# Optimization experiments

Measured on AMD Instinct MI355X. Metric: run time of the kernel, lower is better.

## Reference

```python
import jax, jax.numpy as jnp
from jax import lax
import numpy as np

B, DIM, H, W = 4, 64, 256, 256
HEADS = 8
# (pad_h, pad_w) for kernels (1,7),(1,11),(1,21),(7,1),(11,1),(21,1)
PADS = [(0, 3), (0, 5), (0, 10), (3, 0), (5, 0), (10, 0)]
KSHAPES = [(1, 7), (1, 11), (1, 21), (7, 1), (11, 1), (21, 1)]


def _ln(x, w, b):
    # LayerNorm over channel dim per pixel (torch does it in 'b (h w) c' layout)
    mu = jnp.mean(x, axis=1, keepdims=True)
    var = jnp.mean((x - mu) ** 2, axis=1, keepdims=True)  # unbiased=False
    return (x - mu) / jnp.sqrt(var + 1e-5) * w[None, :, None, None] + b[None, :, None, None]


def _dw(x, k, b, pad):
    # depthwise conv, k: (dim, 1, kh, kw)
    y = lax.conv_general_dilated(
        x, k, window_strides=(1, 1),
        padding=[(pad[0], pad[0]), (pad[1], pad[1])],
        feature_group_count=k.shape[0],
        dimension_numbers=('NCHW', 'OIHW', 'NCHW'))
    return y + b[None, :, None, None]


def _pw(x, w, b):
    # 1x1 conv
    return jnp.einsum('oc,bchw->bohw', w, x) + b[None, :, None, None]


def _l2n(x):
    # torch F.normalize(dim=-1): x / max(||x||_2, 1e-12)
    n = jnp.sqrt(jnp.sum(x * x, axis=-1, keepdims=True))
    return x / jnp.maximum(n, 1e-12)


def _to_attn(t, b, h, w, cph):
    # 'b (head c) h w -> b head w (h c)'  (h slow, c fast in last dim)
    t = t.reshape(b, HEADS, cph, h, w)
    return t.transpose(0, 1, 4, 3, 2).reshape(b, HEADS, w, h * cph)


def setup_inputs() -> dict:
    key = jax.random.key(0)
    keys = jax.random.split(key, 16)
    inp = {
        'x1': jax.random.normal(keys[0], (B, DIM, H, W), jnp.float32),
        'x2': jax.random.normal(keys[1], (B, DIM, H, W), jnp.float32),
        'ln1_w': jnp.ones((DIM,), jnp.float32),
        'ln1_b': jnp.zeros((DIM,), jnp.float32),
        'ln2_w': jnp.ones((DIM,), jnp.float32),
        'ln2_b': jnp.zeros((DIM,), jnp.float32),
        'b_dw': jnp.zeros((12, DIM), jnp.float32),
        'w_pw': 0.05 * jax.random.normal(keys[2], (DIM, DIM), jnp.float32),
        'b_pw': jnp.zeros((DIM,), jnp.float32),
    }
    names = ['k11', 'k12', 'k13', 'k14', 'k15', 'k16',
             'k21', 'k22', 'k23', 'k24', 'k25', 'k26']
    for i, nm in enumerate(names):
        kh, kw = KSHAPES[i % 6]
        inp[nm] = 0.1 * jax.random.normal(keys[3 + i], (DIM, 1, kh, kw), jnp.float32)
    return inp


def reference(x1, x2, ln1_w, ln1_b, ln2_w, ln2_b,
              k11, k12, k13, k14, k15, k16,
              k21, k22, k23, k24, k25, k26,
              b_dw, w_pw, b_pw):
    b, c, h, w = x2.shape
    cph = c // HEADS
    x1n = _ln(x1, ln1_w, ln1_b)
    x2n = _ln(x2, ln2_w, ln2_b)
    ks1 = (k11, k12, k13, k14, k15, k16)
    ks2 = (k21, k22, k23, k24, k25, k26)
    out1 = sum(_dw(x1n, k, b_dw[i], PADS[i]) for i, k in enumerate(ks1))
    out2 = sum(_dw(x2n, k, b_dw[6 + i], PADS[i]) for i, k in enumerate(ks2))
    out1 = _pw(out1, w_pw, b_pw)  # shared 1x1 conv (same weights for both)
    out2 = _pw(out2, w_pw, b_pw)
    q = _l2n(_to_attn(out1, b, h, w, cph))   # (b, head, w, h*cph)
    kk = _l2n(_to_attn(out2, b, h, w, cph))
    v = _to_attn(out2, b, h, w, cph)
    attn = jax.nn.softmax(jnp.einsum('bnwd,bnvd->bnwv', q, kk), axis=-1)
    out4 = jnp.einsum('bnwv,bnvd->bnwd', attn, v) + q
    out4 = out4.reshape(b, HEADS, w, h, cph).transpose(0, 1, 4, 3, 2).reshape(b, c, h, w)
    # note: torch rebinds x1/x2 to normalized tensors before the residual add
    return _pw(out4, w_pw, b_pw) + x1n + x2n
```

## Files before the change

### kernel.cpp

```cpp
#include <hip/hip_runtime.h>

#define HW 65536

typedef __bf16 bf16x8 __attribute__((ext_vector_type(8)));
typedef float f32x4 __attribute__((ext_vector_type(4)));

__device__ __forceinline__ float b2f(unsigned short u) {
    return __uint_as_float(((unsigned)u) << 16);
}
__device__ __forceinline__ unsigned short f2bu(float f) {
    unsigned u = __float_as_uint(f);
    return (unsigned short)((u + 0x7FFFu + ((u >> 16) & 1u)) >> 16);
}
__device__ __forceinline__ void up2(unsigned u, float& lo, float& hi) {
    lo = __uint_as_float(u << 16);
    hi = __uint_as_float(u & 0xFFFF0000u);
}

__global__ void k_prep(const float* k11, const float* k12, const float* k13,
                       const float* k14, const float* k15, const float* k16,
                       const float* k21, const float* k22, const float* k23,
                       const float* k24, const float* k25, const float* k26,
                       const float* bdw, float* wcomb, float* bias) {
    int c = threadIdx.x;
    if (c >= 64) return;
    float* wh1 = wcomb;
    float* wv1 = wcomb + 1344;
    float* wh2 = wcomb + 2688;
    float* wv2 = wcomb + 4032;
    for (int j = 0; j < 21; j++) {
        wh1[c*21+j] = k13[c*21+j];
        wv1[c*21+j] = k16[c*21+j];
        wh2[c*21+j] = k23[c*21+j];
        wv2[c*21+j] = k26[c*21+j];
    }
    for (int j = 0; j < 11; j++) {
        wh1[c*21+j+5] += k12[c*11+j];
        wv1[c*21+j+5] += k15[c*11+j];
        wh2[c*21+j+5] += k22[c*11+j];
        wv2[c*21+j+5] += k25[c*11+j];
    }
    for (int j = 0; j < 7; j++) {
        wh1[c*21+j+7] += k11[c*7+j];
        wv1[c*21+j+7] += k14[c*7+j];
        wh2[c*21+j+7] += k21[c*7+j];
        wv2[c*21+j+7] += k24[c*7+j];
    }
    float s1 = 0.f, s2 = 0.f;
    for (int i = 0; i < 6; i++) { s1 += bdw[i*64+c]; s2 += bdw[(6+i)*64+c]; }
    bias[c] = s1; bias[64+c] = s2;
}

__global__ __launch_bounds__(256) void k_ln(
        const float* __restrict__ x1, const float* __restrict__ x2,
        const float* __restrict__ w1, const float* __restrict__ b1,
        const float* __restrict__ w2, const float* __restrict__ b2,
        unsigned short* __restrict__ o1, unsigned short* __restrict__ o2,
        unsigned short* __restrict__ s12) {
    int p = blockIdx.x * 256 + threadIdx.x;
    int b = p >> 16, hw = p & (HW - 1);
    size_t base = (size_t)b * 64 * HW + hw;
    float v[64];
    unsigned n1[32];
    {
        float s = 0.f;
        #pragma unroll
        for (int c = 0; c < 64; c++) { v[c] = x1[base + (size_t)c * HW]; s += v[c]; }
        float mu = s * 0.015625f, s2 = 0.f;
        #pragma unroll
        for (int c = 0; c < 64; c++) { float d = v[c] - mu; s2 += d * d; }
        float rstd = rsqrtf(s2 * 0.015625f + 1e-5f);
        #pragma unroll
        for (int c2 = 0; c2 < 32; c2++) {
            unsigned short lo = f2bu((v[2*c2]   - mu) * rstd * w1[2*c2]   + b1[2*c2]);
            unsigned short hi = f2bu((v[2*c2+1] - mu) * rstd * w1[2*c2+1] + b1[2*c2+1]);
            o1[base + (size_t)(2*c2)   * HW] = lo;
            o1[base + (size_t)(2*c2+1) * HW] = hi;
            n1[c2] = (unsigned)lo | ((unsigned)hi << 16);
        }
    }
    {
        float s = 0.f;
        #pragma unroll
        for (int c = 0; c < 64; c++) { v[c] = x2[base + (size_t)c * HW]; s += v[c]; }
        float mu = s * 0.015625f, s2 = 0.f;
        #pragma unroll
        for (int c = 0; c < 64; c++) { float d = v[c] - mu; s2 += d * d; }
        float rstd = rsqrtf(s2 * 0.015625f + 1e-5f);
        #pragma unroll
        for (int c2 = 0; c2 < 32; c2++) {
            float a2 = (v[2*c2]   - mu) * rstd * w2[2*c2]   + b2[2*c2];
            float b2n = (v[2*c2+1] - mu) * rstd * w2[2*c2+1] + b2[2*c2+1];
            o2[base + (size_t)(2*c2)   * HW] = f2bu(a2);
            o2[base + (size_t)(2*c2+1) * HW] = f2bu(b2n);
            float lo, hi;
            up2(n1[c2], lo, hi);
            s12[base + (size_t)(2*c2)   * HW] = f2bu(lo + a2);
            s12[base + (size_t)(2*c2+1) * HW] = f2bu(hi + b2n);
        }
    }
}

__global__ __launch_bounds__(256) void k_dw(
        const unsigned short* __restrict__ in1, const unsigned short* __restrict__ in2,
        const float* __restrict__ wcomb, const float* __restrict__ bias,
        unsigned short* __restrict__ o1, unsigned short* __restrict__ o2) {
    __shared__ __align__(16) unsigned short tile[52][288];
    int which = blockIdx.y;
    const unsigned short* in = which ? in2 : in1;
    unsigned short* o = which ? o2 : o1;
    int bx = blockIdx.x;
    int bc = bx >> 3, tileid = bx & 7;
    int c = bc & 63;
    int h0 = tileid * 32;
    const float* whp = wcomb + which * 2688 + c * 21;
    const float* wvp = whp + 1344;
    float wh[21], wv[21];
    #pragma unroll
    for (int j = 0; j < 21; j++) { wh[j] = whp[j]; wv[j] = wvp[j]; }
    float bs = bias[which * 64 + c];
    const unsigned short* src = in + (size_t)bc * HW;
    int tid = threadIdx.x;

    for (int idx = tid; idx < 52 * 36; idx += 256) {
        int row = idx / 36, chunk = idx - row * 36;
        int grow = h0 - 10 + row;
        uint4 val = make_uint4(0u, 0u, 0u, 0u);
        if ((unsigned)grow < 256u && chunk >= 2 && chunk <= 33)
            val = *(const uint4*)(src + grow * 256 + (chunk - 2) * 8);
        *(uint4*)&tile[row][chunk * 8] = val;
    }
    __syncthreads();

    int seg = tid & 31, rgrp = tid >> 5;
    int w0 = seg * 8;
    int r0 = rgrp * 4;

    float acc[4][8];
    #pragma unroll
    for (int k = 0; k < 4; k++)
        #pragma unroll
        for (int i = 0; i < 8; i++) acc[k][i] = bs;

    #pragma unroll
    for (int rr = 0; rr < 24; rr++) {
        uint4 u = *(const uint4*)&tile[r0 + rr][16 + w0];
        float v[8];
        up2(u.x, v[0], v[1]); up2(u.y, v[2], v[3]);
        up2(u.z, v[4], v[5]); up2(u.w, v[6], v[7]);
        #pragma unroll
        for (int k = 0; k < 4; k++) {
            const int j = rr - k;
            if (j >= 0 && j < 21) {
                float wt = wv[j];
                #pragma unroll
                for (int i = 0; i < 8; i++) acc[k][i] += wt * v[i];
            }
        }
    }

    #pragma unroll
    for (int k = 0; k < 4; k++) {
        const unsigned short* rowp = &tile[r0 + k + 10][w0 + 4];
        float hv[32];
        #pragma unroll
        for (int q = 0; q < 8; q++) {
            uint2 u = *(const uint2*)(rowp + q * 4);
            up2(u.x, hv[q*4+0], hv[q*4+1]);
            up2(u.y, hv[q*4+2], hv[q*4+3]);
        }
        #pragma unroll
        for (int j = 0; j < 21; j++) {
            float wt = wh[j];
            #pragma unroll
            for (int i = 0; i < 8; i++) acc[k][i] += wt * hv[i + j + 2];
        }
    }

    size_t obase = (size_t)bc * HW;
    #pragma unroll
    for (int k = 0; k < 4; k++) {
        uint4 u;
        u.x = (unsigned)f2bu(acc[k][0]) | ((unsigned)f2bu(acc[k][1]) << 16);
        u.y = (unsigned)f2bu(acc[k][2]) | ((unsigned)f2bu(acc[k][3]) << 16);
        u.z = (unsigned)f2bu(acc[k][4]) | ((unsigned)f2bu(acc[k][5]) << 16);
        u.w = (unsigned)f2bu(acc[k][6]) | ((unsigned)f2bu(acc[k][7]) << 16);
        *(uint4*)(o + obase + (size_t)(h0 + r0 + k) * 256 + w0) = u;
    }
}

__global__ __launch_bounds__(256) void k_pw(
        const unsigned short* __restrict__ in1, const unsigned short* __restrict__ in2,
        const float* __restrict__ wpw, const float* __restrict__ bpw,
        unsigned short* __restrict__ Eq, unsigned short* __restrict__ Fk,
        unsigned short* __restrict__ Fv) {
    __shared__ __align__(16) unsigned short Ws[64][72];
    __shared__ __align__(16) unsigned short Xs[64][260];
    __shared__ float sb[64];
    int tid = threadIdx.x;
    for (int i = tid; i < 4096; i += 256) Ws[i >> 6][i & 63] = f2bu(wpw[i]);
    if (tid < 64) sb[tid] = bpw[tid];
    int which = blockIdx.y;
    const unsigned short* in = which ? in2 : in1;
    int bx = blockIdx.x;
    int b = bx & 3;
    int h = ((bx >> 2) & 31) * 8 + (bx >> 7);
    const unsigned short* src = in + (size_t)b * 64 * HW + h * 256;
    for (int i = tid; i < 2048; i += 256) {
        int c = i >> 5, ch = i & 31;
        uint4 u = *(const uint4*)(src + (size_t)c * HW + ch * 8);
        *(uint2*)&Xs[c][ch * 8]     = make_uint2(u.x, u.y);
        *(uint2*)&Xs[c][ch * 8 + 4] = make_uint2(u.z, u.w);
    }
    __syncthreads();

    int lane = tid & 63, wv = tid >> 6;
    int rA = lane & 15, g = lane >> 4;
    int p_off = wv * 64;

    f32x4 acc[4][4];
    #pragma unroll
    for (int m = 0; m < 4; m++)
        #pragma unroll
        for (int n = 0; n < 4; n++) acc[m][n] = (f32x4){0.f, 0.f, 0.f, 0.f};

    #pragma unroll
    for (int ks = 0; ks < 2; ks++) {
        int c0 = ks * 32;
        bf16x8 a[4], bb[4];
        #pragma unroll
        for (int m = 0; m < 4; m++)
            a[m] = *(const bf16x8*)&Ws[16 * m + rA][c0 + 8 * g];
        #pragma unroll
        for (int n = 0; n < 4; n++) {
            int p = p_off + 16 * n + rA;
            uint4 bu;
            bu.x = (unsigned)Xs[c0 + 8*g + 0][p] | ((unsigned)Xs[c0 + 8*g + 1][p] << 16);
            bu.y = (unsigned)Xs[c0 + 8*g + 2][p] | ((unsigned)Xs[c0 + 8*g + 3][p] << 16);
            bu.z = (unsigned)Xs[c0 + 8*g + 4][p] | ((unsigned)Xs[c0 + 8*g + 5][p] << 16);
            bu.w = (unsigned)Xs[c0 + 8*g + 6][p] | ((unsigned)Xs[c0 + 8*g + 7][p] << 16);
            bb[n] = *(bf16x8*)&bu;
        }
        #pragma unroll
        for (int m = 0; m < 4; m++)
            #pragma unroll
            for (int n = 0; n < 4; n++)
                acc[m][n] = __builtin_amdgcn_mfma_f32_16x16x32_bf16(a[m], bb[n], acc[m][n], 0, 0, 0);
    }

    unsigned short* dst = which ? Fk : Eq;
    size_t b8 = (size_t)b * 8;
    #pragma unroll
    for (int m = 0; m < 4; m++) {
        int o0 = 16 * m + 4 * g;
        int hd = o0 >> 3, cp = o0 & 7;
        #pragma unroll
        for (int n = 0; n < 4; n++) {
            int p = p_off + 16 * n + rA;
            ushort4 pk;
            #pragma unroll
            for (int r = 0; r < 4; r++)
                ((unsigned short*)&pk)[r] = f2bu(acc[m][n][r] + sb[o0 + r]);
            *(ushort4*)(dst + ((b8 + hd) * 256 + p) * 2048 + h * 8 + cp) = pk;
            if (which) {
                #pragma unroll
                for (int r = 0; r < 4; r++) {
                    int o = o0 + r;
                    Fv[((b8 + (o >> 3)) * 2048 + h * 8 + (o & 7)) * 256 + p] =
                        ((unsigned short*)&pk)[r];
                }
            }
        }
    }
}

__global__ __launch_bounds__(256) void k_norm(
        const unsigned short* __restrict__ Eq, const unsigned short* __restrict__ Fk,
        float* __restrict__ invQ, float* __restrict__ invK) {
    int lane = threadIdx.x & 63, wid = threadIdx.x >> 6;
    int row = blockIdx.x * 4 + wid;
    const unsigned short* src = (row < 8192) ? Eq : Fk;
    int r = row & 8191;
    const unsigned short* p = src + (size_t)r * 2048;
    float s = 0.f;
    #pragma unroll
    for (int it = 0; it < 4; it++) {
        uint4 u = *(const uint4*)(p + it * 512 + lane * 8);
        unsigned vals[4] = {u.x, u.y, u.z, u.w};
        #pragma unroll
        for (int e = 0; e < 4; e++) {
            float lo = b2f((unsigned short)(vals[e] & 0xffffu));
            float hi = b2f((unsigned short)(vals[e] >> 16));
            s += lo * lo + hi * hi;
        }
    }
    #pragma unroll
    for (int m = 1; m < 64; m <<= 1) s += __shfl_xor(s, m, 64);
    if (lane == 0) {
        float inv = 1.f / fmaxf(sqrtf(s), 1e-12f);
        (row < 8192 ? invQ : invK)[r] = inv;
    }
}

__global__ __launch_bounds__(512, 4) void k_qkt(
        const unsigned short* __restrict__ Eq, const unsigned short* __restrict__ Fk,
        float* __restrict__ Sp) {
    int bx = blockIdx.x;
    int bh = bx & 31, t2 = bx >> 5;
    int itile = t2 >> 1, ks = t2 & 1;
    int i0 = itile * 32;
    const unsigned short* Q  = Eq + (size_t)bh * 524288 + ks * 1024;
    const unsigned short* Kp = Fk + (size_t)bh * 524288 + ks * 1024;
    int tid = threadIdx.x, lane = tid & 63, wid = tid >> 6;
    int rA = lane & 15, g = lane >> 4, kf = g * 8;

    f32x4 acc[2][2];
    #pragma unroll
    for (int ib = 0; ib < 2; ib++)
        #pragma unroll
        for (int jb = 0; jb < 2; jb++) acc[ib][jb] = (f32x4){0.f, 0.f, 0.f, 0.f};

    const unsigned short* q0  = Q  + (size_t)(i0 + rA) * 2048 + kf;
    const unsigned short* q1  = q0 + 16 * 2048;
    const unsigned short* kr0 = Kp + (size_t)(wid * 32 + rA) * 2048 + kf;
    const unsigned short* kr1 = kr0 + 16 * 2048;
    for (int k0 = 0; k0 < 1024; k0 += 128) {
        bf16x8 a0[4], a1[4], b0[4], b1[4];
        #pragma unroll
        for (int s = 0; s < 4; s++) {
            int kk = k0 + s * 32;
            a0[s] = *(const bf16x8*)(q0 + kk);
            a1[s] = *(const bf16x8*)(q1 + kk);
            b0[s] = *(const bf16x8*)(kr0 + kk);
            b1[s] = *(const bf16x8*)(kr1 + kk);
        }
        #pragma unroll
        for (int s = 0; s < 4; s++) {
            acc[0][0] = __builtin_amdgcn_mfma_f32_16x16x32_bf16(a0[s], b0[s], acc[0][0], 0, 0, 0);
            acc[1][0] = __builtin_amdgcn_mfma_f32_16x16x32_bf16(a1[s], b0[s], acc[1][0], 0, 0, 0);
            acc[0][1] = __builtin_amdgcn_mfma_f32_16x16x32_bf16(a0[s], b1[s], acc[0][1], 0, 0, 0);
            acc[1][1] = __builtin_amdgcn_mfma_f32_16x16x32_bf16(a1[s], b1[s], acc[1][1], 0, 0, 0);
        }
    }
    float* Sb = Sp + (size_t)(ks * 32 + bh) * 65536 + (size_t)i0 * 256;
    #pragma unroll
    for (int ib = 0; ib < 2; ib++)
        #pragma unroll
        for (int jb = 0; jb < 2; jb++)
            #pragma unroll
            for (int r = 0; r < 4; r++)
                Sb[(ib * 16 + g * 4 + r) * 256 + wid * 32 + jb * 16 + rA] = acc[ib][jb][r];
}

__global__ __launch_bounds__(256) void k_smx(
        const float* __restrict__ Sp, const float* __restrict__ invQ,
        const float* __restrict__ invK, unsigned short* __restrict__ P) {
    __shared__ float sKv[256];
    int bx = blockIdx.x;
    int bh = bx & 31, rg = bx >> 5;
    int tid = threadIdx.x;
    sKv[tid] = invK[bh * 256 + tid];
    __syncthreads();
    int lr = tid >> 5, sub = tid & 31;
    int i = rg * 8 + lr;
    int R = bh * 256 + i;
    const float* p0 = Sp + (size_t)bh * 65536 + i * 256;
    const float* p1 = Sp + (size_t)(32 + bh) * 65536 + i * 256;
    float qs = invQ[R];
    int c0 = sub * 8;
    float4 a0 = *(const float4*)(p0 + c0), a1 = *(const float4*)(p0 + c0 + 4);
    float4 b0 = *(const float4*)(p1 + c0), b1 = *(const float4*)(p1 + c0 + 4);
    float v[8];
    v[0] = (a0.x + b0.x); v[1] = (a0.y + b0.y); v[2] = (a0.z + b0.z); v[3] = (a0.w + b0.w);
    v[4] = (a1.x + b1.x); v[5] = (a1.y + b1.y); v[6] = (a1.z + b1.z); v[7] = (a1.w + b1.w);
    float m = -1e30f;
    #pragma unroll
    for (int e = 0; e < 8; e++) {
        v[e] *= qs * sKv[c0 + e];
        m = fmaxf(m, v[e]);
    }
    #pragma unroll
    for (int msk = 1; msk < 32; msk <<= 1) m = fmaxf(m, __shfl_xor(m, msk, 32));
    float s = 0.f;
    #pragma unroll
    for (int e = 0; e < 8; e++) { v[e] = __expf(v[e] - m); s += v[e]; }
    #pragma unroll
    for (int msk = 1; msk < 32; msk <<= 1) s += __shfl_xor(s, msk, 32);
    float inv = 1.f / s;
    uint4 w;
    w.x = (unsigned)f2bu(v[0] * inv) | ((unsigned)f2bu(v[1] * inv) << 16);
    w.y = (unsigned)f2bu(v[2] * inv) | ((unsigned)f2bu(v[3] * inv) << 16);
    w.z = (unsigned)f2bu(v[4] * inv) | ((unsigned)f2bu(v[5] * inv) << 16);
    w.w = (unsigned)f2bu(v[6] * inv) | ((unsigned)f2bu(v[7] * inv) << 16);
    *(uint4*)(P + (size_t)R * 256 + c0) = w;
}

__global__ __launch_bounds__(512, 4) void k_pv(
        const unsigned short* __restrict__ P, const unsigned short* __restrict__ Fv,
        const unsigned short* __restrict__ Eq, const float* __restrict__ invQ,
        unsigned short* __restrict__ G) {
    __shared__ __align__(16) unsigned short Pb[32][256];
    __shared__ __align__(16) unsigned short Qs[32][1024];
    __shared__ float sQ[32];
    int bx = blockIdx.x;
    int bh = bx & 31, t2 = bx >> 5;
    int itile = t2 >> 1, ds = t2 & 1;
    int i0 = itile * 32;
    int b = bh >> 3, hd = bh & 7;
    const unsigned short* Vt = Fv + (size_t)bh * 524288;
    int tid = threadIdx.x, lane = tid & 63, wid = tid >> 6;
    for (int i = tid; i < 1024; i += 512) {
        int r = i >> 5, cu = i & 31;
        uint4 u = *(const uint4*)(P + (size_t)(bh * 256 + i0 + r) * 256 + cu * 8);
        int su = cu ^ (r & 7);
        *(uint4*)&Pb[r][su * 8] = u;
    }
    for (int i = tid; i < 4096; i += 512) {
        int r = i >> 7, cu = i & 127;
        *(uint4*)&Qs[r][cu * 8] =
            *(const uint4*)(Eq + (size_t)(bh * 256 + i0 + r) * 2048 + ds * 1024 + cu * 8);
    }
    if (tid < 32) sQ[tid] = invQ[bh * 256 + i0 + tid];
    __syncthreads();

    int rA = lane & 15, g = lane >> 4, kf = g * 8;

    bf16x8 pa[2][8];
    #pragma unroll
    for (int ib = 0; ib < 2; ib++)
        #pragma unroll
        for (int ksl = 0; ksl < 8; ksl++) {
            int rr = ib * 16 + rA;
            int unit = (ksl * 4 + g) ^ (rr & 7);
            pa[ib][ksl] = *(const bf16x8*)&Pb[rr][unit * 8];
        }

    int dloc = wid * 128;
    for (int dt = 0; dt < 8; dt++) {
        int dl = dloc + dt * 16;
        int d0 = ds * 1024 + dl;
        const unsigned short* vp = Vt + (size_t)(d0 + rA) * 256 + kf;
        bf16x8 vb[8];
        #pragma unroll
        for (int ksl = 0; ksl < 8; ksl++)
            vb[ksl] = *(const bf16x8*)(vp + ksl * 32);
        f32x4 o0 = {0.f, 0.f, 0.f, 0.f}, o1 = {0.f, 0.f, 0.f, 0.f};
        #pragma unroll
        for (int ksl = 0; ksl < 8; ksl++) {
            o0 = __builtin_amdgcn_mfma_f32_16x16x32_bf16(pa[0][ksl], vb[ksl], o0, 0, 0, 0);
            o1 = __builtin_amdgcn_mfma_f32_16x16x32_bf16(pa[1][ksl], vb[ksl], o1, 0, 0, 0);
        }
        int d = d0 + rA;
        int dlr = dl + rA;
        int cpr = d & 7, hh = d >> 3;
        #pragma unroll
        for (int ib = 0; ib < 2; ib++) {
            f32x4 oa = ib ? o1 : o0;
            int ibase = i0 + ib * 16 + g * 4;
            ushort4 pk;
            #pragma unroll
            for (int r = 0; r < 4; r++) {
                int il = ib * 16 + g * 4 + r;
                float qv = b2f(Qs[il][dlr]) * sQ[il];
                ((unsigned short*)&pk)[r] = f2bu(oa[r] + qv);
            }
            *(ushort4*)(G + (size_t)(b * 64 + hd * 8 + cpr) * HW + hh * 256 + ibase) = pk;
        }
    }
}

__global__ __launch_bounds__(256) void k_final(
        const unsigned short* __restrict__ G, const unsigned short* __restrict__ S12g,
        const float* __restrict__ wpw, const float* __restrict__ bpw,
        float* __restrict__ out) {
    __shared__ __align__(16) unsigned short Ws[64][72];
    __shared__ __align__(16) unsigned short Gs[64][260];
    __shared__ __align__(16) unsigned short S12[64][260];
    __shared__ float sb[64];
    int tid = threadIdx.x;
    for (int i = tid; i < 4096; i += 256) Ws[i >> 6][i & 63] = f2bu(wpw[i]);
    if (tid < 64) sb[tid] = bpw[tid];
    int bx = blockIdx.x, b = bx >> 8, h = bx & 255;
    const unsigned short* src = G + (size_t)b * 64 * HW + h * 256;
    const unsigned short* ssrc = S12g + (size_t)b * 64 * HW + h * 256;
    for (int i = tid; i < 2048; i += 256) {
        int c = i >> 5, ch = i & 31;
        uint4 u = *(const uint4*)(src + (size_t)c * HW + ch * 8);
        *(uint2*)&Gs[c][ch * 8]     = make_uint2(u.x, u.y);
        *(uint2*)&Gs[c][ch * 8 + 4] = make_uint2(u.z, u.w);
        uint4 v = *(const uint4*)(ssrc + (size_t)c * HW + ch * 8);
        *(uint2*)&S12[c][ch * 8]     = make_uint2(v.x, v.y);
        *(uint2*)&S12[c][ch * 8 + 4] = make_uint2(v.z, v.w);
    }
    __syncthreads();

    int lane = tid & 63, wv = tid >> 6;
    int rA = lane & 15, g = lane >> 4;
    int p_off = wv * 64;

    f32x4 acc[4][4];
    #pragma unroll
    for (int m = 0; m < 4; m++)
        #pragma unroll
        for (int n = 0; n < 4; n++) acc[m][n] = (f32x4){0.f, 0.f, 0.f, 0.f};

    #pragma unroll
    for (int ks = 0; ks < 2; ks++) {
        int c0 = ks * 32;
        bf16x8 a[4], bb[4];
        #pragma unroll
        for (int m = 0; m < 4; m++)
            a[m] = *(const bf16x8*)&Ws[16 * m + rA][c0 + 8 * g];
        #pragma unroll
        for (int n = 0; n < 4; n++) {
            int p = p_off + 16 * n + rA;
            uint4 bu;
            bu.x = (unsigned)Gs[c0 + 8*g + 0][p] | ((unsigned)Gs[c0 + 8*g + 1][p] << 16);
            bu.y = (unsigned)Gs[c0 + 8*g + 2][p] | ((unsigned)Gs[c0 + 8*g + 3][p] << 16);
            bu.z = (unsigned)Gs[c0 + 8*g + 4][p] | ((unsigned)Gs[c0 + 8*g + 5][p] << 16);
            bu.w = (unsigned)Gs[c0 + 8*g + 6][p] | ((unsigned)Gs[c0 + 8*g + 7][p] << 16);
            bb[n] = *(bf16x8*)&bu;
        }
        #pragma unroll
        for (int m = 0; m < 4; m++)
            #pragma unroll
            for (int n = 0; n < 4; n++)
                acc[m][n] = __builtin_amdgcn_mfma_f32_16x16x32_bf16(a[m], bb[n], acc[m][n], 0, 0, 0);
    }

    #pragma unroll
    for (int m = 0; m < 4; m++) {
        int o0 = 16 * m + 4 * g;
        #pragma unroll
        for (int n = 0; n < 4; n++) {
            int p = p_off + 16 * n + rA;
            #pragma unroll
            for (int r = 0; r < 4; r++) {
                int o = o0 + r;
                out[(size_t)(b * 64 + o) * HW + h * 256 + p] =
                    acc[m][n][r] + sb[o] + b2f(S12[o][p]);
            }
        }
    }
}

extern "C" void kernel_launch(void* const* d_in, const int* in_sizes, int n_in,
                              void* d_out, int out_size, void* d_ws, size_t ws_size,
                              hipStream_t stream) {
    const float* x1   = (const float*)d_in[0];
    const float* x2   = (const float*)d_in[1];
    const float* ln1w = (const float*)d_in[2];
    const float* ln1b = (const float*)d_in[3];
    const float* ln2w = (const float*)d_in[4];
    const float* ln2b = (const float*)d_in[5];
    const float* bdw  = (const float*)d_in[6];
    const float* wpw  = (const float*)d_in[7];
    const float* bpw  = (const float*)d_in[8];
    const float* kk[12];
    for (int i = 0; i < 12; i++) kk[i] = (const float*)d_in[9 + i];

    char* ws = (char*)d_ws;
    float* wcomb = (float*)ws;
    float* bias  = (float*)(ws + 21504);
    float* invQ  = (float*)(ws + 32768);
    float* invK  = (float*)(ws + 65536);
    const size_t SMALL = 131072;
    const size_t SZ = 33554432;

    unsigned short* S12b = (unsigned short*)(ws + SMALL);
    unsigned short* S1 = (unsigned short*)(ws + SMALL + SZ);
    unsigned short* S2 = (unsigned short*)(ws + SMALL + 2 * SZ);
    unsigned short* S3 = (unsigned short*)(ws + SMALL + 3 * SZ);
    unsigned short* dw1 = (unsigned short*)d_out;
    unsigned short* dw2 = dw1 + SZ / 2;
    float* Sp = (float*)d_out;
    unsigned short* P = (unsigned short*)((char*)d_out + 20971520);

    k_prep<<<1, 64, 0, stream>>>(kk[0], kk[1], kk[2], kk[3], kk[4], kk[5],
                                 kk[6], kk[7], kk[8], kk[9], kk[10], kk[11],
                                 bdw, wcomb, bias);
    k_ln<<<1024, 256, 0, stream>>>(x1, x2, ln1w, ln1b, ln2w, ln2b, S1, S2, S12b);
    k_dw<<<dim3(2048, 2), 256, 0, stream>>>(S1, S2, wcomb, bias, dw1, dw2);
    k_pw<<<dim3(1024, 2), 256, 0, stream>>>(dw1, dw2, wpw, bpw, S1, S2, S3);
    k_norm<<<4096, 256, 0, stream>>>(S1, S2, invQ, invK);
    k_qkt<<<512, 512, 0, stream>>>(S1, S2, Sp);
    k_smx<<<1024, 256, 0, stream>>>(Sp, invQ, invK, P);
    k_pv<<<512, 512, 0, stream>>>(P, S3, S1, invQ, S2);
    k_final<<<1024, 256, 0, stream>>>(S2, S12b, wpw, bpw, (float*)d_out);
}
```

Measured before the change: 321.7 us.

## Recast depthwise strip convolutions as banded-Toeplitz MFMA matmuls with swizzled LDS tile

```diff
diff --git a/kernel.cpp b/kernel.cpp
--- a/kernel.cpp
+++ b/kernel.cpp
@@ -105,7 +105,9 @@
         const unsigned short* __restrict__ in1, const unsigned short* __restrict__ in2,
         const float* __restrict__ wcomb, const float* __restrict__ bias,
         unsigned short* __restrict__ o1, unsigned short* __restrict__ o2) {
-    __shared__ __align__(16) unsigned short tile[52][288];
+    __shared__ __align__(16) unsigned short tileRaw[52 * 320];
+    __shared__ __align__(16) unsigned short ThT[16][64];
+    __shared__ __align__(16) unsigned short TvA[16][64];
     int which = blockIdx.y;
     const unsigned short* in = which ? in2 : in1;
     unsigned short* o = which ? o2 : o1;
@@ -113,79 +115,80 @@
     int bc = bx >> 3, tileid = bx & 7;
     int c = bc & 63;
     int h0 = tileid * 32;
-    const float* whp = wcomb + which * 2688 + c * 21;
-    const float* wvp = whp + 1344;
-    float wh[21], wv[21];
-    #pragma unroll
-    for (int j = 0; j < 21; j++) { wh[j] = whp[j]; wv[j] = wvp[j]; }
-    float bs = bias[which * 64 + c];
+    int tid = threadIdx.x;
+
+    {
+        const float* whp = wcomb + which * 2688 + c * 21;
+        const float* wvp = whp + 1344;
+        for (int i = tid; i < 2048; i += 256) {
+            int mat = i >> 10;
+            int idx = i & 1023;
+            int n = idx >> 6, k = idx & 63;
+            int j = k - n - 6;
+            float v = (j >= 0 && j < 21) ? (mat ? wvp[j] : whp[j]) : 0.f;
+            (mat ? &TvA[0][0] : &ThT[0][0])[idx] = f2bu(v);
+        }
+    }
     const unsigned short* src = in + (size_t)bc * HW;
-    int tid = threadIdx.x;
-
-    for (int idx = tid; idx < 52 * 36; idx += 256) {
-        int row = idx / 36, chunk = idx - row * 36;
+    for (int idx = tid; idx < 52 * 40; idx += 256) {
+        int row = idx / 40, u = idx - row * 40;
         int grow = h0 - 10 + row;
         uint4 val = make_uint4(0u, 0u, 0u, 0u);
-        if ((unsigned)grow < 256u && chunk >= 2 && chunk <= 33)
-            val = *(const uint4*)(src + grow * 256 + (chunk - 2) * 8);
-        *(uint4*)&tile[row][chunk * 8] = val;
-    }
+        if ((unsigned)grow < 256u && u >= 2 && u < 34)
+            val = *(const uint4*)(src + grow * 256 + (u - 2) * 8);
+        *(uint4*)&tileRaw[row * 320 + ((u ^ ((row >> 1) & 7)) << 3)] = val;
+    }
+    float bs = bias[which * 64 + c];
     __syncthreads();
 
-    int seg = tid & 31, rgrp = tid >> 5;
-    int w0 = seg * 8;
-    int r0 = rgrp * 4;
-
-    float acc[4][8];
-    #pragma unroll
-    for (int k = 0; k < 4; k++)
-        #pragma unroll
-        for (int i = 0; i < 8; i++) acc[k][i] = bs;
-
-    #pragma unroll
-    for (int rr = 0; rr < 24; rr++) {
-        uint4 u = *(const uint4*)&tile[r0 + rr][16 + w0];
-        float v[8];
-        up2(u.x, v[0], v[1]); up2(u.y, v[2], v[3]);
-        up2(u.z, v[4], v[5]); up2(u.w, v[6], v[7]);
-        #pragma unroll
-        for (int k = 0; k < 4; k++) {
-            const int j = rr - k;
-            if (j >= 0 && j < 21) {
-                float wt = wv[j];
-                #pragma unroll
-                for (int i = 0; i < 8; i++) acc[k][i] += wt * v[i];
-            }
-        }
-    }
-
-    #pragma unroll
-    for (int k = 0; k < 4; k++) {
-        const unsigned short* rowp = &tile[r0 + k + 10][w0 + 4];
-        float hv[32];
-        #pragma unroll
-        for (int q = 0; q < 8; q++) {
-            uint2 u = *(const uint2*)(rowp + q * 4);
-            up2(u.x, hv[q*4+0], hv[q*4+1]);
-            up2(u.y, hv[q*4+2], hv[q*4+3]);
-        }
-        #pragma unroll
-        for (int j = 0; j < 21; j++) {
-            float wt = wh[j];
-            #pragma unroll
-            for (int i = 0; i < 8; i++) acc[k][i] += wt * hv[i + j + 2];
-        }
-    }
-
-    size_t obase = (size_t)bc * HW;
-    #pragma unroll
-    for (int k = 0; k < 4; k++) {
-        uint4 u;
-        u.x = (unsigned)f2bu(acc[k][0]) | ((unsigned)f2bu(acc[k][1]) << 16);
-        u.y = (unsigned)f2bu(acc[k][2]) | ((unsigned)f2bu(acc[k][3]) << 16);
-        u.z = (unsigned)f2bu(acc[k][4]) | ((unsigned)f2bu(acc[k][5]) << 16);
-        u.w = (unsigned)f2bu(acc[k][6]) | ((unsigned)f2bu(acc[k][7]) << 16);
-        *(uint4*)(o + obase + (size_t)(h0 + r0 + k) * 256 + w0) = u;
+    int lane = tid & 63, wid = tid >> 6;
+    int rA = lane & 15, g = lane >> 4, kf = g * 8;
+
+    bf16x8 thB0 = *(const bf16x8*)&ThT[rA][kf];
+    bf16x8 thB1 = *(const bf16x8*)&ThT[rA][32 + kf];
+    bf16x8 tvA0 = *(const bf16x8*)&TvA[rA][kf];
+    bf16x8 tvA1 = *(const bf16x8*)&TvA[rA][32 + kf];
+
+    int ht = wid & 1, wgrp = wid >> 1;
+    for (int t = 0; t < 8; t++) {
+        int w0 = (wgrp * 8 + t) * 16;
+        int ub = w0 >> 3;
+        int hrow = ht * 16 + rA + 10;
+        int xh = (hrow >> 1) & 7;
+        bf16x8 ax0 = *(const bf16x8*)&tileRaw[hrow * 320 + (((ub + g) ^ xh) << 3)];
+        bf16x8 ax1 = *(const bf16x8*)&tileRaw[hrow * 320 + (((ub + 4 + g) ^ xh) << 3)];
+        int uvb = ub + 2 + (rA >> 3);
+        int el = rA & 7;
+        uint4 bv0, bv1;
+        unsigned* pv0 = (unsigned*)&bv0;
+        unsigned* pv1 = (unsigned*)&bv1;
+        #pragma unroll
+        for (int e2 = 0; e2 < 4; e2++) {
+            int k0i = kf + 2 * e2;
+            int r0 = ht * 16 + k0i - 6;  r0 = r0 < 0 ? 0 : (r0 > 51 ? 51 : r0);
+            int r1 = ht * 16 + k0i - 5;  r1 = r1 < 0 ? 0 : (r1 > 51 ? 51 : r1);
+            unsigned lo = tileRaw[r0 * 320 + ((uvb ^ ((r0 >> 1) & 7)) << 3) + el];
+            unsigned hi = tileRaw[r1 * 320 + ((uvb ^ ((r1 >> 1) & 7)) << 3) + el];
+            pv0[e2] = lo | (hi << 16);
+            int k1i = 32 + kf + 2 * e2;
+            int r2 = ht * 16 + k1i - 6;  r2 = r2 < 0 ? 0 : (r2 > 51 ? 51 : r2);
+            int r3 = ht * 16 + k1i - 5;  r3 = r3 < 0 ? 0 : (r3 > 51 ? 51 : r3);
+            unsigned lo2 = tileRaw[r2 * 320 + ((uvb ^ ((r2 >> 1) & 7)) << 3) + el];
+            unsigned hi2 = tileRaw[r3 * 320 + ((uvb ^ ((r3 >> 1) & 7)) << 3) + el];
+            pv1[e2] = lo2 | (hi2 << 16);
+        }
+        f32x4 acc = {bs, bs, bs, bs};
+        acc = __builtin_amdgcn_mfma_f32_16x16x32_bf16(ax0, thB0, acc, 0, 0, 0);
+        acc = __builtin_amdgcn_mfma_f32_16x16x32_bf16(ax1, thB1, acc, 0, 0, 0);
+        acc = __builtin_amdgcn_mfma_f32_16x16x32_bf16(tvA0, *(bf16x8*)&bv0, acc, 0, 0, 0);
+        acc = __builtin_amdgcn_mfma_f32_16x16x32_bf16(tvA1, *(bf16x8*)&bv1, acc, 0, 0, 0);
+        int wc = w0 + rA;
+        size_t obase = (size_t)bc * HW + wc;
+        #pragma unroll
+        for (int r = 0; r < 4; r++) {
+            int hh = h0 + ht * 16 + 4 * g + r;
+            o[obase + (size_t)hh * 256] = f2bu(acc[r]);
+        }
     }
 }
 
```

Measured after the change: 307.8 us. -4.3%, faster.
